# Performance work log

Measured on AMD Instinct MI355X. Metric: run time of the kernel, lower is better.

The kernel has to match this reference:

```python
import jax, jax.numpy as jnp
import numpy as np

N_NODES = 100000
N_EDGES = 1600000
F_IN = 128
HID = 128
N_GRAPHS = 64


def setup_inputs() -> dict:
    key = jax.random.key(0)
    ks = jax.random.split(key, 12)
    x = jax.random.normal(ks[0], (N_NODES, F_IN), dtype=jnp.float32)
    edge_index = jax.random.randint(ks[1], (2, N_EDGES), 0, N_NODES, dtype=jnp.int32)
    batch = jnp.sort(jax.random.randint(ks[2], (N_NODES,), 0, N_GRAPHS, dtype=jnp.int32))
    s = 1.0 / np.sqrt(F_IN)
    W1 = jax.random.normal(ks[3], (F_IN, HID), dtype=jnp.float32) * s
    b1 = jnp.zeros((HID,), jnp.float32)
    W2 = jax.random.normal(ks[4], (HID, HID), dtype=jnp.float32) * s
    b2 = jnp.zeros((HID,), jnp.float32)
    W3 = jax.random.normal(ks[5], (HID, HID), dtype=jnp.float32) * s
    b3 = jnp.zeros((HID,), jnp.float32)
    Wc1 = jax.random.normal(ks[6], (HID, HID // 2), dtype=jnp.float32) * s
    bc1 = jnp.zeros((HID // 2,), jnp.float32)
    Wc2 = jax.random.normal(ks[7], (HID // 2, 1), dtype=jnp.float32) * (1.0 / np.sqrt(HID // 2))
    bc2 = jnp.zeros((1,), jnp.float32)
    return {"x": x, "edge_index": edge_index, "batch": batch,
            "W1": W1, "b1": b1, "W2": W2, "b2": b2, "W3": W3, "b3": b3,
            "Wc1": Wc1, "bc1": bc1, "Wc2": Wc2, "bc2": bc2}


def _gcn_conv(x, W, b, src, dst, norm, n_nodes):
    # PyG GCNConv: x' = D^-1/2 (A+I) D^-1/2 (x W) + b  (self-loops already in src/dst)
    h = x @ W                                   # [N, H] small GEMM
    msg = h[src] * norm[:, None]                # [E+N, H] gather (memory bound)
    out = jax.ops.segment_sum(msg, dst, num_segments=n_nodes)  # scatter-add
    return out + b


def reference(x, edge_index, batch, W1, b1, W2, b2, W3, b3, Wc1, bc1, Wc2, bc2):
    n = x.shape[0]
    loop = jnp.arange(n, dtype=edge_index.dtype)
    src = jnp.concatenate([edge_index[0], loop])
    dst = jnp.concatenate([edge_index[1], loop])
    deg = jax.ops.segment_sum(jnp.ones_like(dst, dtype=x.dtype), dst, num_segments=n)
    dinv = jax.lax.rsqrt(jnp.maximum(deg, 1.0))
    norm = dinv[src] * dinv[dst]                # [E+N]

    h = jax.nn.elu(_gcn_conv(x, W1, b1, src, dst, norm, n))   # dropout is identity in eval
    h = jax.nn.elu(_gcn_conv(h, W2, b2, src, dst, norm, n))
    h = jax.nn.elu(_gcn_conv(h, W3, b3, src, dst, norm, n))

    # global mean pool over graphs
    sums = jax.ops.segment_sum(h, batch, num_segments=N_GRAPHS)
    cnts = jax.ops.segment_sum(jnp.ones((n,), h.dtype), batch, num_segments=N_GRAPHS)
    g = sums / jnp.maximum(cnts, 1.0)[:, None]  # [G, H]

    z = jax.nn.relu(g @ Wc1 + bc1)
    logits = z @ Wc2 + bc2
    return jax.nn.sigmoid(logits)               # [G, 1]
```

## Files before the change

kernel.cpp:

```cpp
#include <hip/hip_runtime.h>
#include <cstdint>
#include <cstddef>


#define SUBCAP 512
#define CSRCAP 4608
#define TILE 4096

typedef __attribute__((ext_vector_type(8))) short short8;
typedef __attribute__((ext_vector_type(4))) float f32x4;
typedef __attribute__((ext_vector_type(2))) _Float16 h16x2;

__device__ __forceinline__ float bf2f(uint32_t u) {
  return __uint_as_float(u << 16);
}
__device__ __forceinline__ uint32_t f2bf(float f) {
  uint32_t x = __float_as_uint(f);
  return (x + 0x7FFFu + ((x >> 16) & 1u)) >> 16;
}

union H16 { _Float16 h; uint16_t u; };
union H2U { h16x2 h; uint32_t u; };

__device__ __forceinline__ uint32_t f2e5m2(float f) {
  f = fminf(fmaxf(f, -30000.f), 30000.f);
  H16 cv;
  cv.h = (_Float16)f;
  uint32_t h = cv.u;
  uint32_t r = h + 0x7Fu + ((h >> 8) & 1u);
  return (r >> 8) & 0xFFu;
}

__device__ __forceinline__ float e5m2f(uint32_t b) {
  H16 cv;
  cv.u = (uint16_t)(b << 8);
  return (float)cv.h;
}


__global__ __launch_bounds__(256) void bucket_scatter(const int* __restrict__ src,
                                                      const int* __restrict__ dst,
                                                      int* __restrict__ bcur,
                                                      uint32_t* __restrict__ ebuf,
                                                      int nE, int nbuk) {
  uint32_t xcc;
  asm("s_getreg_b32 %0, hwreg(HW_REG_XCC_ID)" : "=s"(xcc));
  __shared__ int lhist[1024];
  __shared__ int gbase[1024];
  int t = threadIdx.x;
  for (int i = t; i < nbuk; i += 256) lhist[i] = 0;
  __syncthreads();

  int e0 = blockIdx.x * TILE;
  int myd[16], mys[16], myrank[16];
#pragma unroll
  for (int j = 0; j < 16; ++j) {
    int e = e0 + t + j * 256;
    if (e < nE) {
      int d = dst[e];
      myd[j] = d;
      mys[j] = src[e];
      myrank[j] = atomicAdd(&lhist[d >> 7], 1);
    } else {
      myd[j] = -1;
    }
  }
  __syncthreads();
  for (int i = t; i < nbuk; i += 256) {
    int c = lhist[i];
    gbase[i] = c ? atomicAdd(&bcur[((i << 3) | (int)xcc) * 16], c) : 0;
  }
  __syncthreads();
#pragma unroll
  for (int j = 0; j < 16; ++j) {
    if (myd[j] >= 0) {
      int b = myd[j] >> 7;
      int pos = gbase[b] + myrank[j];
      if (pos < SUBCAP) {
        int sub = (b << 3) | (int)xcc;
        ebuf[(size_t)sub * SUBCAP + pos] =
            ((uint32_t)(myd[j] & 127) << 20) | (uint32_t)mys[j];
      }
    }
  }
}

__global__ __launch_bounds__(256) void bucket_build(const uint32_t* __restrict__ ebuf,
                                                    const int* __restrict__ bcur,
                                                    int* __restrict__ deg,
                                                    float* __restrict__ dinv,
                                                    int* __restrict__ offs,
                                                    int* __restrict__ csr,
                                                    const float* __restrict__ W1,
                                                    const float* __restrict__ W2,
                                                    const float* __restrict__ W3,
                                                    uint16_t* __restrict__ WT,
                                                    float* __restrict__ pool,
                                                    int n, int nbuk) {
  int b = blockIdx.x;
  int base = b << 7;
  __shared__ int hist[128];
  __shared__ int pre[128];
  __shared__ int lcur[128];
  int t = threadIdx.x;

  for (int id = b * 256 + t; id < 3 * 16384; id += nbuk * 256) {
    int w = id >> 14;
    int rem = id & 16383;
    int k = rem >> 7, nn = rem & 127;
    const float* W = (w == 0) ? W1 : ((w == 1) ? W2 : W3);
    WT[w * 16384 + nn * 128 + k] = (uint16_t)f2bf(W[k * 128 + nn]);
  }
  for (int id = b * 256 + t; id < 64 * 128; id += nbuk * 256) pool[id] = 0.f;

  if (t < 128) hist[t] = 0;
  __syncthreads();
  int cnts[8];
#pragma unroll
  for (int x = 0; x < 8; ++x) {
    int sub = (b << 3) | x;
    int cnt = min(bcur[sub * 16], SUBCAP);
    cnts[x] = cnt;
    const uint32_t* eb = ebuf + (size_t)sub * SUBCAP;
    for (int e = t; e < cnt; e += 256) atomicAdd(&hist[eb[e] >> 20], 1);
  }
  __syncthreads();
  if (t < 128) pre[t] = (hist[t] + 3) & ~3;
  __syncthreads();
  for (int d = 1; d < 128; d <<= 1) {
    int v = (t >= d && t < 128) ? pre[t - d] : 0;
    __syncthreads();
    if (t < 128) pre[t] += v;
    __syncthreads();
  }
  if (t < 128) {
    int dg = hist[t];
    int start = b * CSRCAP + pre[t] - ((dg + 3) & ~3);
    lcur[t] = start;
    if (base + t < n) {
      deg[base + t] = dg;
      dinv[base + t] = rsqrtf((float)(dg + 1));
      offs[base + t] = start;
    }
  }
  __syncthreads();
#pragma unroll
  for (int x = 0; x < 8; ++x) {
    int sub = (b << 3) | x;
    int cnt = cnts[x];
    const uint32_t* eb = ebuf + (size_t)sub * SUBCAP;
    for (int e = t; e < cnt; e += 256) {
      uint32_t ed = eb[e];
      int pos = atomicAdd(&lcur[ed >> 20], 1);
      csr[pos] = (int)((ed & 0xFFFFFu) << 7);
    }
  }
}


template <bool F32IN>
__global__ __launch_bounds__(256) void gemm_mfma(const uint16_t* __restrict__ Xb,
                                                 const float* __restrict__ X32,
                                                 const uint16_t* __restrict__ WTb,
                                                 const float* __restrict__ dinv,
                                                 uint8_t* __restrict__ tab, int n) {
  __shared__ uint16_t sW[128 * 136];
  int t = threadIdx.x;
#pragma unroll
  for (int i = 0; i < 8; ++i) {
    int j = t + i * 256;
    int r = j >> 4, c = j & 15;
    float4 v = ((const float4*)WTb)[j];
    *(float4*)(sW + r * 136 + c * 8) = v;
  }
  __syncthreads();

  int wave = t >> 6, lane = t & 63;
  int quad = lane >> 4, l15 = lane & 15;
  int m = blockIdx.x * 64 + wave * 16 + l15;
  int mm = min(m, n - 1);

  short8 a[4];
#pragma unroll
  for (int kc = 0; kc < 4; ++kc) {
    if constexpr (F32IN) {
      const float* p = X32 + (size_t)mm * 128 + kc * 32 + quad * 8;
      float4 lo = *(const float4*)p;
      float4 hi = *(const float4*)(p + 4);
      a[kc] = (short8){(short)f2bf(lo.x), (short)f2bf(lo.y),
                       (short)f2bf(lo.z), (short)f2bf(lo.w),
                       (short)f2bf(hi.x), (short)f2bf(hi.y),
                       (short)f2bf(hi.z), (short)f2bf(hi.w)};
    } else {
      a[kc] = *(const short8*)(Xb + (size_t)mm * 128 + kc * 32 + quad * 8);
    }
  }

  f32x4 acc[8];
#pragma unroll
  for (int nn = 0; nn < 8; ++nn) acc[nn] = (f32x4){0.f, 0.f, 0.f, 0.f};

#pragma unroll
  for (int nn = 0; nn < 8; ++nn) {
    int nrow = nn * 16 + l15;
#pragma unroll
    for (int kc = 0; kc < 4; ++kc) {
      short8 b = *(const short8*)(sW + nrow * 136 + kc * 32 + quad * 8);
      acc[nn] = __builtin_amdgcn_mfma_f32_16x16x32_bf16(a[kc], b, acc[nn], 0, 0, 0);
    }
  }

  int mrow = blockIdx.x * 64 + wave * 16 + quad * 4;
#pragma unroll
  for (int r = 0; r < 4; ++r) {
    int row = mrow + r;
    if (row < n) {
      float dn = dinv[row];
#pragma unroll
      for (int nn = 0; nn < 8; ++nn) {
        tab[(size_t)row * 128 + nn * 16 + l15] = (uint8_t)f2e5m2(acc[nn][r] * dn);
      }
    }
  }
}


__device__ __forceinline__ void acc_pk(uint32_t u, h16x2& a01, h16x2& a23) {
  H2U p01, p23;
  p01.u = __builtin_amdgcn_perm(u, 0u, 0x05010400u);
  p23.u = __builtin_amdgcn_perm(u, 0u, 0x07010600u);
  a01 += p01.h;
  a23 += p23.h;
}

template <bool POOL>
__global__ __launch_bounds__(512) void gather_gemm(const uint8_t* __restrict__ tab,
                                                   const int* __restrict__ csr,
                                                   const int* __restrict__ offs,
                                                   const int* __restrict__ deg,
                                                   const float* __restrict__ dinv,
                                                   const float* __restrict__ b,
                                                   const uint16_t* __restrict__ WTb,
                                                   uint8_t* __restrict__ tabN,
                                                   const int* __restrict__ batch,
                                                   float* __restrict__ pool,
                                                   int n) {
  __shared__ uint16_t sW[POOL ? 8 : 128 * 136];
  __shared__ uint16_t sA[16 * 136];
  __shared__ int sb[16];
  int t = threadIdx.x;
  int blk = (int)blockIdx.x;

  if constexpr (!POOL) {
#pragma unroll
    for (int i = 0; i < 4; ++i) {
      int j = t + i * 512;
      int r = j >> 4, c = j & 15;
      float4 v = ((const float4*)WTb)[j];
      *(float4*)(sW + r * 136 + c * 8) = v;
    }
  } else {
    if (t < 16) sb[t] = batch[min(blk * 16 + t, n - 1)];
  }

  int hw = t >> 5;
  int node = min(blk * 16 + hw, n - 1);
  int l = t & 31;
  int c = l * 4;
  const uint8_t* tabc = tab + c;
  int e0 = offs[node];
  int e1 = e0 + deg[node];
  h16x2 a01 = (h16x2){(_Float16)0.f, (_Float16)0.f};
  h16x2 a23 = (h16x2){(_Float16)0.f, (_Float16)0.f};

  int e = e0;
  for (; e + 7 < e1; e += 8) {
    int4 ca = *(const int4*)(csr + e);
    int4 cb = *(const int4*)(csr + e + 4);
    uint32_t u[8];
    u[0] = *(const uint32_t*)(tabc + ca.x);
    u[1] = *(const uint32_t*)(tabc + ca.y);
    u[2] = *(const uint32_t*)(tabc + ca.z);
    u[3] = *(const uint32_t*)(tabc + ca.w);
    u[4] = *(const uint32_t*)(tabc + cb.x);
    u[5] = *(const uint32_t*)(tabc + cb.y);
    u[6] = *(const uint32_t*)(tabc + cb.z);
    u[7] = *(const uint32_t*)(tabc + cb.w);
#pragma unroll
    for (int j = 0; j < 8; ++j) acc_pk(u[j], a01, a23);
  }
  if (e + 3 < e1) {
    int4 ca = *(const int4*)(csr + e);
    uint32_t u[4];
    u[0] = *(const uint32_t*)(tabc + ca.x);
    u[1] = *(const uint32_t*)(tabc + ca.y);
    u[2] = *(const uint32_t*)(tabc + ca.z);
    u[3] = *(const uint32_t*)(tabc + ca.w);
#pragma unroll
    for (int j = 0; j < 4; ++j) acc_pk(u[j], a01, a23);
    e += 4;
  }
  for (; e < e1; ++e) acc_pk(*(const uint32_t*)(tabc + csr[e]), a01, a23);

  float a0 = (float)a01.x, a1 = (float)a01.y;
  float a2 = (float)a23.x, a3 = (float)a23.y;

  float dn = dinv[node];
  uint32_t uh = *(const uint32_t*)(tabc + node * 128);
  float4 bb = *(const float4*)(b + c);
  float o0 = (a0 + e5m2f(uh & 0xFFu)) * dn + bb.x;
  float o1 = (a1 + e5m2f((uh >> 8) & 0xFFu)) * dn + bb.y;
  float o2 = (a2 + e5m2f((uh >> 16) & 0xFFu)) * dn + bb.z;
  float o3 = (a3 + e5m2f(uh >> 24)) * dn + bb.w;
  o0 = o0 > 0.f ? o0 : expm1f(o0);
  o1 = o1 > 0.f ? o1 : expm1f(o1);
  o2 = o2 > 0.f ? o2 : expm1f(o2);
  o3 = o3 > 0.f ? o3 : expm1f(o3);
  uint2 po;
  po.x = f2bf(o0) | (f2bf(o1) << 16);
  po.y = f2bf(o2) | (f2bf(o3) << 16);
  *(uint2*)(sA + hw * 136 + c) = po;
  __syncthreads();

  if constexpr (POOL) {
    if (t < 128) {
      int base = blk * 16;
      int iend = min(16, n - base);
      float acc = 0.f;
      int cur = sb[0];
      for (int i = 0; i < iend; ++i) {
        int g = sb[i];
        if (g != cur) {
          atomicAdd(&pool[cur * 128 + t], acc);
          acc = 0.f;
          cur = g;
        }
        acc += bf2f((uint32_t)sA[i * 136 + t]);
      }
      atomicAdd(&pool[cur * 128 + t], acc);
    }
  } else {
    int wave = t >> 6, lane = t & 63;
    int quad = lane >> 4, l15 = lane & 15;
    f32x4 acc = (f32x4){0.f, 0.f, 0.f, 0.f};
#pragma unroll
    for (int kc = 0; kc < 4; ++kc) {
      short8 av = *(const short8*)(sA + l15 * 136 + kc * 32 + quad * 8);
      short8 bv = *(const short8*)(sW + (wave * 16 + l15) * 136 + kc * 32 + quad * 8);
      acc = __builtin_amdgcn_mfma_f32_16x16x32_bf16(av, bv, acc, 0, 0, 0);
    }
    int mrow = blk * 16 + quad * 4;
#pragma unroll
    for (int r = 0; r < 4; ++r) {
      int row = mrow + r;
      if (row < n) {
        float dno = dinv[row];
        tabN[(size_t)row * 128 + wave * 16 + l15] = (uint8_t)f2e5m2(acc[r] * dno);
      }
    }
  }
}


__global__ __launch_bounds__(64) void classifier_kernel(const float* __restrict__ pool,
                                                        const int* __restrict__ batch,
                                                        const float* __restrict__ Wc1,
                                                        const float* __restrict__ bc1,
                                                        const float* __restrict__ Wc2,
                                                        const float* __restrict__ bc2,
                                                        float* __restrict__ out, int n) {
  int g = blockIdx.x;
  int j = threadIdx.x;
  __shared__ float sg[128];

  int lo = 0, hi = n;
  while (lo < hi) {
    int mid = (lo + hi) >> 1;
    if (batch[mid] < g) lo = mid + 1; else hi = mid;
  }
  int a = lo;
  lo = 0; hi = n;
  while (lo < hi) {
    int mid = (lo + hi) >> 1;
    if (batch[mid] < g + 1) lo = mid + 1; else hi = mid;
  }
  float inv = 1.f / (float)max(lo - a, 1);

  sg[j] = pool[g * 128 + j] * inv;
  sg[j + 64] = pool[g * 128 + j + 64] * inv;
  __syncthreads();

  float acc = bc1[j];
#pragma unroll 4
  for (int k = 0; k < 128; ++k) acc += sg[k] * Wc1[k * 64 + j];
  float z = fmaxf(acc, 0.f);

  float v = z * Wc2[j];
#pragma unroll
  for (int m = 32; m > 0; m >>= 1) v += __shfl_xor(v, m, 64);
  if (j == 0) out[g] = 1.f / (1.f + expf(-(v + bc2[0])));
}

extern "C" void kernel_launch(void* const* d_in, const int* in_sizes, int n_in,
                              void* d_out, int out_size, void* d_ws, size_t ws_size,
                              hipStream_t stream) {
  const float* x   = (const float*)d_in[0];
  const int* ei    = (const int*)d_in[1];
  const int* batch = (const int*)d_in[2];
  const float* W1  = (const float*)d_in[3];
  const float* b1  = (const float*)d_in[4];
  const float* W2  = (const float*)d_in[5];
  const float* b2  = (const float*)d_in[6];
  const float* W3  = (const float*)d_in[7];
  const float* b3  = (const float*)d_in[8];
  const float* Wc1 = (const float*)d_in[9];
  const float* bc1 = (const float*)d_in[10];
  const float* Wc2 = (const float*)d_in[11];
  const float* bc2 = (const float*)d_in[12];

  int n  = in_sizes[2];
  int nE = in_sizes[1] / 2;
  const int* src = ei;
  const int* dst = ei + nE;
  int nbuk = (n + 127) >> 7;

  uint8_t*  tab0 = (uint8_t*)d_ws;
  uint8_t*  tab1 = tab0 + (size_t)n * 128;
  float* dinv    = (float*)(tab0 + (size_t)n * 128 + (size_t)n * 256);
  int*   deg     = (int*)(dinv + n);
  int*   offs    = deg + n;
  int*   bcur    = offs + n + 4;
  int*   csr     = bcur + nbuk * 8 * 16;
  uint32_t* ebuf = (uint32_t*)(csr + (size_t)nbuk * CSRCAP);
  uint16_t* WT   = (uint16_t*)(ebuf + (size_t)nbuk * 8 * SUBCAP);
  float* pool    = (float*)(WT + 3 * 16384);
  float* out     = (float*)d_out;

  hipMemsetAsync(bcur, 0, (size_t)nbuk * 8 * 16 * sizeof(int), stream);
  bucket_scatter<<<(nE + TILE - 1) / TILE, 256, 0, stream>>>(src, dst, bcur, ebuf, nE, nbuk);
  bucket_build<<<nbuk, 256, 0, stream>>>(ebuf, bcur, deg, dinv, offs, csr,
                                         W1, W2, W3, WT, pool, n, nbuk);

  int gfb = (n + 15) / 16;
  gemm_mfma<true><<<(n + 63) / 64, 256, 0, stream>>>(nullptr, x, WT, dinv, tab0, n);
  gather_gemm<false><<<gfb, 512, 0, stream>>>(tab0, csr, offs, deg, dinv, b1,
                                              WT + 16384, tab1, nullptr, nullptr, n);
  gather_gemm<false><<<gfb, 512, 0, stream>>>(tab1, csr, offs, deg, dinv, b2,
                                              WT + 32768, tab0, nullptr, nullptr, n);
  gather_gemm<true><<<gfb, 512, 0, stream>>>(tab0, csr, offs, deg, dinv, b3,
                                             nullptr, nullptr, batch, pool, n);
  classifier_kernel<<<64, 64, 0, stream>>>(pool, batch, Wc1, bc1, Wc2, bc2, out, n);
}
```

Baseline: 336.3 us.

## Split each node's edge gather across two half-waves with shuffle reduction

Each block now handles 8 nodes instead of 16, and each node gets a full 64-lane wave. The two 32-lane halves each gather half of the node's edges and combine their partial sums with a cross-half shuffle. The goal is shorter per-node serial gather chains and more memory parallelism. In exchange, the grid doubles, so the 128x136 weight tile is loaded into LDS twice as often, and half of the 16-row MFMA output is wasted on zero-padded rows.

```diff
diff --git a/kernel.cpp b/kernel.cpp
--- a/kernel.cpp
+++ b/kernel.cpp
@@ -247,7 +247,7 @@
                                                    int n) {
   __shared__ uint16_t sW[POOL ? 8 : 128 * 136];
   __shared__ uint16_t sA[16 * 136];
-  __shared__ int sb[16];
+  __shared__ int sb[8];
   int t = threadIdx.x;
   int blk = (int)blockIdx.x;
 
@@ -259,22 +259,33 @@
       float4 v = ((const float4*)WTb)[j];
       *(float4*)(sW + r * 136 + c * 8) = v;
     }
+    for (int i = t; i < 8 * 136; i += 512) sA[8 * 136 + i] = 0;
   } else {
-    if (t < 16) sb[t] = batch[min(blk * 16 + t, n - 1)];
-  }
-
-  int hw = t >> 5;
-  int node = min(blk * 16 + hw, n - 1);
-  int l = t & 31;
+    if (t < 8) sb[t] = batch[min(blk * 8 + t, n - 1)];
+  }
+
+  int wv = t >> 6;
+  int lane = t & 63;
+  int g = lane >> 5;
+  int l = lane & 31;
+  int node = min(blk * 8 + wv, n - 1);
   int c = l * 4;
   const uint8_t* tabc = tab + c;
+
+  int dg = deg[node];
   int e0 = offs[node];
-  int e1 = e0 + deg[node];
+  int e1 = e0 + dg;
+  int half4 = (((dg + 1) >> 1) + 3) & ~3;
+  int emid = e0 + half4;
+  if (emid > e1) emid = e1;
+  int myb = g ? emid : e0;
+  int mye = g ? e1 : emid;
+
   h16x2 a01 = (h16x2){(_Float16)0.f, (_Float16)0.f};
   h16x2 a23 = (h16x2){(_Float16)0.f, (_Float16)0.f};
 
-  int e = e0;
-  for (; e + 7 < e1; e += 8) {
+  int e = myb;
+  for (; e + 7 < mye; e += 8) {
     int4 ca = *(const int4*)(csr + e);
     int4 cb = *(const int4*)(csr + e + 4);
     uint32_t u[8];
@@ -289,7 +300,7 @@
 #pragma unroll
     for (int j = 0; j < 8; ++j) acc_pk(u[j], a01, a23);
   }
-  if (e + 3 < e1) {
+  if (e + 3 < mye) {
     int4 ca = *(const int4*)(csr + e);
     uint32_t u[4];
     u[0] = *(const uint32_t*)(tabc + ca.x);
@@ -300,7 +311,15 @@
     for (int j = 0; j < 4; ++j) acc_pk(u[j], a01, a23);
     e += 4;
   }
-  for (; e < e1; ++e) acc_pk(*(const uint32_t*)(tabc + csr[e]), a01, a23);
+  for (; e < mye; ++e) acc_pk(*(const uint32_t*)(tabc + csr[e]), a01, a23);
+
+  H2U x01, x23, y01, y23;
+  x01.h = a01;
+  x23.h = a23;
+  y01.u = (uint32_t)__shfl_xor((int)x01.u, 32, 64);
+  y23.u = (uint32_t)__shfl_xor((int)x23.u, 32, 64);
+  a01 = x01.h + y01.h;
+  a23 = x23.h + y23.h;
 
   float a0 = (float)a01.x, a1 = (float)a01.y;
   float a2 = (float)a23.x, a3 = (float)a23.y;
@@ -316,31 +335,33 @@
   o1 = o1 > 0.f ? o1 : expm1f(o1);
   o2 = o2 > 0.f ? o2 : expm1f(o2);
   o3 = o3 > 0.f ? o3 : expm1f(o3);
-  uint2 po;
-  po.x = f2bf(o0) | (f2bf(o1) << 16);
-  po.y = f2bf(o2) | (f2bf(o3) << 16);
-  *(uint2*)(sA + hw * 136 + c) = po;
+  if (g == 0) {
+    uint2 po;
+    po.x = f2bf(o0) | (f2bf(o1) << 16);
+    po.y = f2bf(o2) | (f2bf(o3) << 16);
+    *(uint2*)(sA + wv * 136 + c) = po;
+  }
   __syncthreads();
 
   if constexpr (POOL) {
     if (t < 128) {
-      int base = blk * 16;
-      int iend = min(16, n - base);
+      int base = blk * 8;
+      int iend = min(8, n - base);
       float acc = 0.f;
       int cur = sb[0];
       for (int i = 0; i < iend; ++i) {
-        int g = sb[i];
-        if (g != cur) {
+        int gg = sb[i];
+        if (gg != cur) {
           atomicAdd(&pool[cur * 128 + t], acc);
           acc = 0.f;
-          cur = g;
+          cur = gg;
         }
         acc += bf2f((uint32_t)sA[i * 136 + t]);
       }
       atomicAdd(&pool[cur * 128 + t], acc);
     }
   } else {
-    int wave = t >> 6, lane = t & 63;
+    int wave = t >> 6;
     int quad = lane >> 4, l15 = lane & 15;
     f32x4 acc = (f32x4){0.f, 0.f, 0.f, 0.f};
 #pragma unroll
@@ -349,13 +370,15 @@
       short8 bv = *(const short8*)(sW + (wave * 16 + l15) * 136 + kc * 32 + quad * 8);
       acc = __builtin_amdgcn_mfma_f32_16x16x32_bf16(av, bv, acc, 0, 0, 0);
     }
-    int mrow = blk * 16 + quad * 4;
-#pragma unroll
-    for (int r = 0; r < 4; ++r) {
-      int row = mrow + r;
-      if (row < n) {
-        float dno = dinv[row];
-        tabN[(size_t)row * 128 + wave * 16 + l15] = (uint8_t)f2e5m2(acc[r] * dno);
+    if (quad < 2) {
+      int mrow = blk * 8 + quad * 4;
+#pragma unroll
+      for (int r = 0; r < 4; ++r) {
+        int row = mrow + r;
+        if (row < n) {
+          float dno = dinv[row];
+          tabN[(size_t)row * 128 + wave * 16 + l15] = (uint8_t)f2e5m2(acc[r] * dno);
+        }
       }
     }
   }
@@ -441,7 +464,7 @@
   bucket_build<<<nbuk, 256, 0, stream>>>(ebuf, bcur, deg, dinv, offs, csr,
                                          W1, W2, W3, WT, pool, n, nbuk);
 
-  int gfb = (n + 15) / 16;
+  int gfb = (n + 7) / 8;
   gemm_mfma<true><<<(n + 63) / 64, 256, 0, stream>>>(nullptr, x, WT, dinv, tab0, n);
   gather_gemm<false><<<gfb, 512, 0, stream>>>(tab0, csr, offs, deg, dinv, b1,
                                               WT + 16384, tab1, nullptr, nullptr, n);
```

After: 436.7 us. 1.3x slower.

## Process nodes in degree-sorted order within graphs and unroll gather by 16

Applied to the files above, without the earlier changes.

Builds a node permutation that groups nodes by graph and then by in-degree, using a 64x64 histogram, a single-block scan and an atomic scatter. The gather kernels walk nodes through this permutation, so the 16 half-waves in a block see similar edge counts and wait less on the longest node. Keeping the graph as the outer key keeps the pooled segments contiguous. The gather loop is also unrolled to 16 edges for more memory-level parallelism. This adds two small kernels, an extra memset and an indirect lookup per node, and output writes are no longer sequential.

```diff
diff --git a/kernel.cpp b/kernel.cpp
--- a/kernel.cpp
+++ b/kernel.cpp
@@ -87,6 +87,7 @@
 
 __global__ __launch_bounds__(256) void bucket_build(const uint32_t* __restrict__ ebuf,
                                                     const int* __restrict__ bcur,
+                                                    const int* __restrict__ batch,
                                                     int* __restrict__ deg,
                                                     float* __restrict__ dinv,
                                                     int* __restrict__ offs,
@@ -96,6 +97,7 @@
                                                     const float* __restrict__ W3,
                                                     uint16_t* __restrict__ WT,
                                                     float* __restrict__ pool,
+                                                    int* __restrict__ dhist,
                                                     int n, int nbuk) {
   int b = blockIdx.x;
   int base = b << 7;
@@ -141,6 +143,7 @@
       deg[base + t] = dg;
       dinv[base + t] = rsqrtf((float)(dg + 1));
       offs[base + t] = start;
+      atomicAdd(&dhist[batch[base + t] * 64 + min(dg, 63)], 1);
     }
   }
   __syncthreads();
@@ -154,6 +157,39 @@
       int pos = atomicAdd(&lcur[ed >> 20], 1);
       csr[pos] = (int)((ed & 0xFFFFFu) << 7);
     }
+  }
+}
+
+__global__ __launch_bounds__(1024) void deg_scan(int* __restrict__ dhist) {
+  __shared__ int s[1024];
+  int t = threadIdx.x;
+  int4 v = ((int4*)dhist)[t];
+  int sum = v.x + v.y + v.z + v.w;
+  s[t] = sum;
+  __syncthreads();
+  for (int d = 1; d < 1024; d <<= 1) {
+    int w = (t >= d) ? s[t - d] : 0;
+    __syncthreads();
+    s[t] += w;
+    __syncthreads();
+  }
+  int ex = s[t] - sum;
+  int4 o;
+  o.x = ex;
+  o.y = ex + v.x;
+  o.z = ex + v.x + v.y;
+  o.w = ex + v.x + v.y + v.z;
+  ((int4*)dhist)[t] = o;
+}
+
+__global__ __launch_bounds__(256) void perm_scatter(const int* __restrict__ batch,
+                                                    const int* __restrict__ deg,
+                                                    int* __restrict__ dhist,
+                                                    int* __restrict__ perm, int n) {
+  int i = blockIdx.x * 256 + threadIdx.x;
+  if (i < n) {
+    int k = batch[i] * 64 + min(deg[i], 63);
+    perm[atomicAdd(&dhist[k], 1)] = i;
   }
 }
 
@@ -244,6 +280,7 @@
                                                    uint8_t* __restrict__ tabN,
                                                    const int* __restrict__ batch,
                                                    float* __restrict__ pool,
+                                                   const int* __restrict__ perm,
                                                    int n) {
   __shared__ uint16_t sW[POOL ? 8 : 128 * 136];
   __shared__ uint16_t sA[16 * 136];
@@ -260,11 +297,11 @@
       *(float4*)(sW + r * 136 + c * 8) = v;
     }
   } else {
-    if (t < 16) sb[t] = batch[min(blk * 16 + t, n - 1)];
+    if (t < 16) sb[t] = batch[perm[min(blk * 16 + t, n - 1)]];
   }
 
   int hw = t >> 5;
-  int node = min(blk * 16 + hw, n - 1);
+  int node = perm[min(blk * 16 + hw, n - 1)];
   int l = t & 31;
   int c = l * 4;
   const uint8_t* tabc = tab + c;
@@ -274,7 +311,32 @@
   h16x2 a23 = (h16x2){(_Float16)0.f, (_Float16)0.f};
 
   int e = e0;
-  for (; e + 7 < e1; e += 8) {
+  for (; e + 15 < e1; e += 16) {
+    int4 c0 = *(const int4*)(csr + e);
+    int4 c1 = *(const int4*)(csr + e + 4);
+    int4 c2 = *(const int4*)(csr + e + 8);
+    int4 c3 = *(const int4*)(csr + e + 12);
+    uint32_t u[16];
+    u[0]  = *(const uint32_t*)(tabc + c0.x);
+    u[1]  = *(const uint32_t*)(tabc + c0.y);
+    u[2]  = *(const uint32_t*)(tabc + c0.z);
+    u[3]  = *(const uint32_t*)(tabc + c0.w);
+    u[4]  = *(const uint32_t*)(tabc + c1.x);
+    u[5]  = *(const uint32_t*)(tabc + c1.y);
+    u[6]  = *(const uint32_t*)(tabc + c1.z);
+    u[7]  = *(const uint32_t*)(tabc + c1.w);
+    u[8]  = *(const uint32_t*)(tabc + c2.x);
+    u[9]  = *(const uint32_t*)(tabc + c2.y);
+    u[10] = *(const uint32_t*)(tabc + c2.z);
+    u[11] = *(const uint32_t*)(tabc + c2.w);
+    u[12] = *(const uint32_t*)(tabc + c3.x);
+    u[13] = *(const uint32_t*)(tabc + c3.y);
+    u[14] = *(const uint32_t*)(tabc + c3.z);
+    u[15] = *(const uint32_t*)(tabc + c3.w);
+#pragma unroll
+    for (int j = 0; j < 16; ++j) acc_pk(u[j], a01, a23);
+  }
+  if (e + 7 < e1) {
     int4 ca = *(const int4*)(csr + e);
     int4 cb = *(const int4*)(csr + e + 4);
     uint32_t u[8];
@@ -288,6 +350,7 @@
     u[7] = *(const uint32_t*)(tabc + cb.w);
 #pragma unroll
     for (int j = 0; j < 8; ++j) acc_pk(u[j], a01, a23);
+    e += 8;
   }
   if (e + 3 < e1) {
     int4 ca = *(const int4*)(csr + e);
@@ -352,8 +415,9 @@
     int mrow = blk * 16 + quad * 4;
 #pragma unroll
     for (int r = 0; r < 4; ++r) {
-      int row = mrow + r;
-      if (row < n) {
+      int ri = mrow + r;
+      if (ri < n) {
+        int row = perm[ri];
         float dno = dinv[row];
         tabN[(size_t)row * 128 + wave * 16 + l15] = (uint8_t)f2e5m2(acc[r] * dno);
       }
@@ -426,6 +490,8 @@
 
   uint8_t*  tab0 = (uint8_t*)d_ws;
   uint8_t*  tab1 = tab0 + (size_t)n * 128;
+  int*   perm    = (int*)(tab0 + (size_t)n * 256);
+  int*   dhist   = perm + n;
   float* dinv    = (float*)(tab0 + (size_t)n * 128 + (size_t)n * 256);
   int*   deg     = (int*)(dinv + n);
   int*   offs    = deg + n;
@@ -437,17 +503,20 @@
   float* out     = (float*)d_out;
 
   hipMemsetAsync(bcur, 0, (size_t)nbuk * 8 * 16 * sizeof(int), stream);
+  hipMemsetAsync(dhist, 0, 4096 * sizeof(int), stream);
   bucket_scatter<<<(nE + TILE - 1) / TILE, 256, 0, stream>>>(src, dst, bcur, ebuf, nE, nbuk);
-  bucket_build<<<nbuk, 256, 0, stream>>>(ebuf, bcur, deg, dinv, offs, csr,
-                                         W1, W2, W3, WT, pool, n, nbuk);
+  bucket_build<<<nbuk, 256, 0, stream>>>(ebuf, bcur, batch, deg, dinv, offs, csr,
+                                         W1, W2, W3, WT, pool, dhist, n, nbuk);
+  deg_scan<<<1, 1024, 0, stream>>>(dhist);
+  perm_scatter<<<(n + 255) / 256, 256, 0, stream>>>(batch, deg, dhist, perm, n);
 
   int gfb = (n + 15) / 16;
   gemm_mfma<true><<<(n + 63) / 64, 256, 0, stream>>>(nullptr, x, WT, dinv, tab0, n);
   gather_gemm<false><<<gfb, 512, 0, stream>>>(tab0, csr, offs, deg, dinv, b1,
-                                              WT + 16384, tab1, nullptr, nullptr, n);
+                                              WT + 16384, tab1, nullptr, nullptr, perm, n);
   gather_gemm<false><<<gfb, 512, 0, stream>>>(tab1, csr, offs, deg, dinv, b2,
-                                              WT + 32768, tab0, nullptr, nullptr, n);
+                                              WT + 32768, tab0, nullptr, nullptr, perm, n);
   gather_gemm<true><<<gfb, 512, 0, stream>>>(tab0, csr, offs, deg, dinv, b3,
-                                             nullptr, nullptr, batch, pool, n);
+                                             nullptr, nullptr, batch, pool, perm, n);
   classifier_kernel<<<64, 64, 0, stream>>>(pool, batch, Wc1, bc1, Wc2, bc2, out, n);
 }
```

Result: slower. 358.5 us (+6.6%).

## Halve gather block threads, widen per-lane loads, read weights from global

Applied to the files above, without the earlier changes.

The gather kernel now uses 16 lanes per node, each loading 8 fp8 bytes per neighbour instead of 4, and launches 256 threads per block instead of 512. The 34 KB shared-memory weight tile is gone. Each wave computes two 16-column MFMA tiles and reads the B operand straight from global or L2. This cuts per-block weight staging and LDS usage, which should allow more blocks per CU, at the cost of uncached-in-LDS weight reads and fewer threads in flight per block.

```diff
diff --git a/kernel.cpp b/kernel.cpp
--- a/kernel.cpp
+++ b/kernel.cpp
@@ -225,16 +225,21 @@
 }
 
 
-__device__ __forceinline__ void acc_pk(uint32_t u, h16x2& a01, h16x2& a23) {
-  H2U p01, p23;
-  p01.u = __builtin_amdgcn_perm(u, 0u, 0x05010400u);
-  p23.u = __builtin_amdgcn_perm(u, 0u, 0x07010600u);
+__device__ __forceinline__ void acc_pk8(uint2 u, h16x2& a01, h16x2& a23,
+                                        h16x2& a45, h16x2& a67) {
+  H2U p01, p23, p45, p67;
+  p01.u = __builtin_amdgcn_perm(u.x, 0u, 0x05010400u);
+  p23.u = __builtin_amdgcn_perm(u.x, 0u, 0x07010600u);
+  p45.u = __builtin_amdgcn_perm(u.y, 0u, 0x05010400u);
+  p67.u = __builtin_amdgcn_perm(u.y, 0u, 0x07010600u);
   a01 += p01.h;
   a23 += p23.h;
+  a45 += p45.h;
+  a67 += p67.h;
 }
 
 template <bool POOL>
-__global__ __launch_bounds__(512) void gather_gemm(const uint8_t* __restrict__ tab,
+__global__ __launch_bounds__(256) void gather_gemm(const uint8_t* __restrict__ tab,
                                                    const int* __restrict__ csr,
                                                    const int* __restrict__ offs,
                                                    const int* __restrict__ deg,
@@ -245,81 +250,86 @@
                                                    const int* __restrict__ batch,
                                                    float* __restrict__ pool,
                                                    int n) {
-  __shared__ uint16_t sW[POOL ? 8 : 128 * 136];
   __shared__ uint16_t sA[16 * 136];
   __shared__ int sb[16];
   int t = threadIdx.x;
   int blk = (int)blockIdx.x;
 
-  if constexpr (!POOL) {
-#pragma unroll
-    for (int i = 0; i < 4; ++i) {
-      int j = t + i * 512;
-      int r = j >> 4, c = j & 15;
-      float4 v = ((const float4*)WTb)[j];
-      *(float4*)(sW + r * 136 + c * 8) = v;
-    }
-  } else {
+  if constexpr (POOL) {
     if (t < 16) sb[t] = batch[min(blk * 16 + t, n - 1)];
   }
 
-  int hw = t >> 5;
-  int node = min(blk * 16 + hw, n - 1);
-  int l = t & 31;
-  int c = l * 4;
+  int grp = t >> 4;
+  int l = t & 15;
+  int node = min(blk * 16 + grp, n - 1);
+  int c = l * 8;
   const uint8_t* tabc = tab + c;
   int e0 = offs[node];
   int e1 = e0 + deg[node];
   h16x2 a01 = (h16x2){(_Float16)0.f, (_Float16)0.f};
-  h16x2 a23 = (h16x2){(_Float16)0.f, (_Float16)0.f};
+  h16x2 a23 = a01, a45 = a01, a67 = a01;
 
   int e = e0;
   for (; e + 7 < e1; e += 8) {
-    int4 ca = *(const int4*)(csr + e);
-    int4 cb = *(const int4*)(csr + e + 4);
-    uint32_t u[8];
-    u[0] = *(const uint32_t*)(tabc + ca.x);
-    u[1] = *(const uint32_t*)(tabc + ca.y);
-    u[2] = *(const uint32_t*)(tabc + ca.z);
-    u[3] = *(const uint32_t*)(tabc + ca.w);
-    u[4] = *(const uint32_t*)(tabc + cb.x);
-    u[5] = *(const uint32_t*)(tabc + cb.y);
-    u[6] = *(const uint32_t*)(tabc + cb.z);
-    u[7] = *(const uint32_t*)(tabc + cb.w);
-#pragma unroll
-    for (int j = 0; j < 8; ++j) acc_pk(u[j], a01, a23);
+    int4 c0 = *(const int4*)(csr + e);
+    int4 c1 = *(const int4*)(csr + e + 4);
+    uint2 u[8];
+    u[0] = *(const uint2*)(tabc + c0.x);
+    u[1] = *(const uint2*)(tabc + c0.y);
+    u[2] = *(const uint2*)(tabc + c0.z);
+    u[3] = *(const uint2*)(tabc + c0.w);
+    u[4] = *(const uint2*)(tabc + c1.x);
+    u[5] = *(const uint2*)(tabc + c1.y);
+    u[6] = *(const uint2*)(tabc + c1.z);
+    u[7] = *(const uint2*)(tabc + c1.w);
+#pragma unroll
+    for (int j = 0; j < 8; ++j) acc_pk8(u[j], a01, a23, a45, a67);
   }
   if (e + 3 < e1) {
-    int4 ca = *(const int4*)(csr + e);
-    uint32_t u[4];
-    u[0] = *(const uint32_t*)(tabc + ca.x);
-    u[1] = *(const uint32_t*)(tabc + ca.y);
-    u[2] = *(const uint32_t*)(tabc + ca.z);
-    u[3] = *(const uint32_t*)(tabc + ca.w);
-#pragma unroll
-    for (int j = 0; j < 4; ++j) acc_pk(u[j], a01, a23);
+    int4 c0 = *(const int4*)(csr + e);
+    uint2 u[4];
+    u[0] = *(const uint2*)(tabc + c0.x);
+    u[1] = *(const uint2*)(tabc + c0.y);
+    u[2] = *(const uint2*)(tabc + c0.z);
+    u[3] = *(const uint2*)(tabc + c0.w);
+#pragma unroll
+    for (int j = 0; j < 4; ++j) acc_pk8(u[j], a01, a23, a45, a67);
     e += 4;
   }
-  for (; e < e1; ++e) acc_pk(*(const uint32_t*)(tabc + csr[e]), a01, a23);
-
-  float a0 = (float)a01.x, a1 = (float)a01.y;
-  float a2 = (float)a23.x, a3 = (float)a23.y;
+  for (; e < e1; ++e)
+    acc_pk8(*(const uint2*)(tabc + csr[e]), a01, a23, a45, a67);
+
+  float f0 = (float)a01.x, f1 = (float)a01.y;
+  float f2 = (float)a23.x, f3 = (float)a23.y;
+  float f4 = (float)a45.x, f5 = (float)a45.y;
+  float f6 = (float)a67.x, f7 = (float)a67.y;
 
   float dn = dinv[node];
-  uint32_t uh = *(const uint32_t*)(tabc + node * 128);
-  float4 bb = *(const float4*)(b + c);
-  float o0 = (a0 + e5m2f(uh & 0xFFu)) * dn + bb.x;
-  float o1 = (a1 + e5m2f((uh >> 8) & 0xFFu)) * dn + bb.y;
-  float o2 = (a2 + e5m2f((uh >> 16) & 0xFFu)) * dn + bb.z;
-  float o3 = (a3 + e5m2f(uh >> 24)) * dn + bb.w;
+  uint2 uh = *(const uint2*)(tabc + node * 128);
+  float4 bb0 = *(const float4*)(b + c);
+  float4 bb1 = *(const float4*)(b + c + 4);
+  float o0 = (f0 + e5m2f(uh.x & 0xFFu)) * dn + bb0.x;
+  float o1 = (f1 + e5m2f((uh.x >> 8) & 0xFFu)) * dn + bb0.y;
+  float o2 = (f2 + e5m2f((uh.x >> 16) & 0xFFu)) * dn + bb0.z;
+  float o3 = (f3 + e5m2f(uh.x >> 24)) * dn + bb0.w;
+  float o4 = (f4 + e5m2f(uh.y & 0xFFu)) * dn + bb1.x;
+  float o5 = (f5 + e5m2f((uh.y >> 8) & 0xFFu)) * dn + bb1.y;
+  float o6 = (f6 + e5m2f((uh.y >> 16) & 0xFFu)) * dn + bb1.z;
+  float o7 = (f7 + e5m2f(uh.y >> 24)) * dn + bb1.w;
   o0 = o0 > 0.f ? o0 : expm1f(o0);
   o1 = o1 > 0.f ? o1 : expm1f(o1);
   o2 = o2 > 0.f ? o2 : expm1f(o2);
   o3 = o3 > 0.f ? o3 : expm1f(o3);
-  uint2 po;
+  o4 = o4 > 0.f ? o4 : expm1f(o4);
+  o5 = o5 > 0.f ? o5 : expm1f(o5);
+  o6 = o6 > 0.f ? o6 : expm1f(o6);
+  o7 = o7 > 0.f ? o7 : expm1f(o7);
+  uint4 po;
   po.x = f2bf(o0) | (f2bf(o1) << 16);
   po.y = f2bf(o2) | (f2bf(o3) << 16);
-  *(uint2*)(sA + hw * 136 + c) = po;
+  po.z = f2bf(o4) | (f2bf(o5) << 16);
+  po.w = f2bf(o6) | (f2bf(o7) << 16);
+  *(uint4*)(sA + grp * 136 + c) = po;
   __syncthreads();
 
   if constexpr (POOL) {
@@ -342,12 +352,18 @@
   } else {
     int wave = t >> 6, lane = t & 63;
     int quad = lane >> 4, l15 = lane & 15;
-    f32x4 acc = (f32x4){0.f, 0.f, 0.f, 0.f};
+    short8 av[4];
+#pragma unroll
+    for (int kc = 0; kc < 4; ++kc)
+      av[kc] = *(const short8*)(sA + l15 * 136 + kc * 32 + quad * 8);
+    f32x4 acc0 = (f32x4){0.f, 0.f, 0.f, 0.f};
+    f32x4 acc1 = (f32x4){0.f, 0.f, 0.f, 0.f};
 #pragma unroll
     for (int kc = 0; kc < 4; ++kc) {
-      short8 av = *(const short8*)(sA + l15 * 136 + kc * 32 + quad * 8);
-      short8 bv = *(const short8*)(sW + (wave * 16 + l15) * 136 + kc * 32 + quad * 8);
-      acc = __builtin_amdgcn_mfma_f32_16x16x32_bf16(av, bv, acc, 0, 0, 0);
+      short8 bv0 = *(const short8*)(WTb + (wave * 32 + l15) * 128 + kc * 32 + quad * 8);
+      acc0 = __builtin_amdgcn_mfma_f32_16x16x32_bf16(av[kc], bv0, acc0, 0, 0, 0);
+      short8 bv1 = *(const short8*)(WTb + (wave * 32 + 16 + l15) * 128 + kc * 32 + quad * 8);
+      acc1 = __builtin_amdgcn_mfma_f32_16x16x32_bf16(av[kc], bv1, acc1, 0, 0, 0);
     }
     int mrow = blk * 16 + quad * 4;
 #pragma unroll
@@ -355,7 +371,8 @@
       int row = mrow + r;
       if (row < n) {
         float dno = dinv[row];
-        tabN[(size_t)row * 128 + wave * 16 + l15] = (uint8_t)f2e5m2(acc[r] * dno);
+        tabN[(size_t)row * 128 + wave * 32 + l15] = (uint8_t)f2e5m2(acc0[r] * dno);
+        tabN[(size_t)row * 128 + wave * 32 + 16 + l15] = (uint8_t)f2e5m2(acc1[r] * dno);
       }
     }
   }
@@ -443,11 +460,11 @@
 
   int gfb = (n + 15) / 16;
   gemm_mfma<true><<<(n + 63) / 64, 256, 0, stream>>>(nullptr, x, WT, dinv, tab0, n);
-  gather_gemm<false><<<gfb, 512, 0, stream>>>(tab0, csr, offs, deg, dinv, b1,
+  gather_gemm<false><<<gfb, 256, 0, stream>>>(tab0, csr, offs, deg, dinv, b1,
                                               WT + 16384, tab1, nullptr, nullptr, n);
-  gather_gemm<false><<<gfb, 512, 0, stream>>>(tab1, csr, offs, deg, dinv, b2,
+  gather_gemm<false><<<gfb, 256, 0, stream>>>(tab1, csr, offs, deg, dinv, b2,
                                               WT + 32768, tab0, nullptr, nullptr, n);
-  gather_gemm<true><<<gfb, 512, 0, stream>>>(tab0, csr, offs, deg, dinv, b3,
+  gather_gemm<true><<<gfb, 256, 0, stream>>>(tab0, csr, offs, deg, dinv, b3,
                                              nullptr, nullptr, batch, pool, n);
   classifier_kernel<<<64, 64, 0, stream>>>(pool, batch, Wc1, bc1, Wc2, bc2, out, n);
 }
```

Measured after the change: 338.8 us. About the same (+0.7%).
